# Kernel optimization log

Hardware: AMD Instinct MI355X
Metric: run time of the kernel (lower is better)

The kernel has to match this reference:

```python
import jax, jax.numpy as jnp
import numpy as np

STEPS = 30
BATCH = 1048576
HIDDEN = 32


def setup_inputs() -> dict:
    key = jax.random.key(0)
    k_s, k_w1, k_b1, k_w2, k_b2 = jax.random.split(key, 5)
    return {
        "S": jax.random.normal(k_s, (BATCH, STEPS), dtype=jnp.float32),
        "W1": jax.random.normal(k_w1, (3, HIDDEN), dtype=jnp.float32) * (1.0 / np.sqrt(3.0)),
        "b1": jax.random.normal(k_b1, (HIDDEN,), dtype=jnp.float32) * 0.01,
        "W2": jax.random.normal(k_w2, (HIDDEN, 1), dtype=jnp.float32) * (1.0 / np.sqrt(HIDDEN)),
        "b2": jax.random.normal(k_b2, (1,), dtype=jnp.float32) * 0.01,
        "a_init": jnp.zeros((1,), dtype=jnp.float32),
    }


def reference(S, W1, b1, W2, b2, a_init):
    B = S.shape[0]
    h0 = jnp.zeros((B, 1), dtype=S.dtype)
    d0 = jnp.broadcast_to(a_init.reshape(1, 1), (B, 1))  # a_init.expand(batch, 1)

    def step(carry, s_t):
        h, d_prev = carry
        x = jnp.concatenate([s_t[:, None], d_prev, h], axis=1)  # (B, 3)
        hidden = jax.nn.relu(x @ W1 + b1)                        # (B, 32)
        d = hidden @ W2 + b2                                     # (B, 1)
        h_new = 0.8 * h + 0.2 * d
        return (h_new, d), d

    # scan over time: S.T has shape (steps, B)
    (_, _), deltas = jax.lax.scan(step, (h0, d0), S.T)
    # deltas: (steps, B, 1) -> (B, steps)
    return jnp.transpose(deltas[:, :, 0], (1, 0))
```

## Files before the change

kernel.cpp:

```cpp
#include <hip/hip_runtime.h>

#define STEPS 30
#define HID 32
#define HALF_H 16
#define TPB 256
#define EPB (TPB / 2)
#define LDS_STRIDE (STEPS + 1)

__global__ __launch_bounds__(TPB, 4) void hedge_kernel(
    const float* __restrict__ S,
    const float* __restrict__ W1,
    const float* __restrict__ b1,
    const float* __restrict__ W2,
    const float* __restrict__ b2,
    const float* __restrict__ a_init,
    float* __restrict__ out)
{
    __shared__ float tile[EPB * LDS_STRIDE];
    const int tid  = threadIdx.x;
    const int half = tid & 1;
    const int el   = tid >> 1;
    const long long base = (long long)blockIdx.x * (EPB * STEPS);

    #pragma unroll
    for (int k = 0; k < (EPB * STEPS) / TPB; ++k) {
        int idx = tid + k * TPB;
        float v = S[base + idx];
        int row = idx / STEPS;
        int col = idx - row * STEPS;
        tile[row * LDS_STRIDE + col] = v;
    }

    const int j0 = half * HALF_H;
    float wa[HALF_H], wc[HALF_H], we[HALF_H], wb[HALF_H], w2[HALF_H];
    #pragma unroll
    for (int q = 0; q < HALF_H / 4; ++q) {
        float4 va = ((const float4*)(W1 + 0 * HID + j0))[q];
        float4 vc = ((const float4*)(W1 + 1 * HID + j0))[q];
        float4 ve = ((const float4*)(W1 + 2 * HID + j0))[q];
        float4 vb = ((const float4*)(b1 + j0))[q];
        float4 v2 = ((const float4*)(W2 + j0))[q];
        wa[4*q+0]=va.x; wa[4*q+1]=va.y; wa[4*q+2]=va.z; wa[4*q+3]=va.w;
        wc[4*q+0]=vc.x; wc[4*q+1]=vc.y; wc[4*q+2]=vc.z; wc[4*q+3]=vc.w;
        we[4*q+0]=ve.x; we[4*q+1]=ve.y; we[4*q+2]=ve.z; we[4*q+3]=ve.w;
        wb[4*q+0]=vb.x; wb[4*q+1]=vb.y; wb[4*q+2]=vb.z; wb[4*q+3]=vb.w;
        w2[4*q+0]=v2.x; w2[4*q+1]=v2.y; w2[4*q+2]=v2.z; w2[4*q+3]=v2.w;
    }
    const float bias2 = b2[0];
    float d = a_init[0];
    float h = 0.0f;
    __syncthreads();

    float* my = &tile[el * LDS_STRIDE];
    #pragma unroll
    for (int t = 0; t < STEPS; ++t) {
        const float s = my[t];
        float a0 = 0.f, a1 = 0.f, a2 = 0.f, a3 = 0.f;
        #pragma unroll
        for (int j = 0; j < HALF_H; j += 4) {
            float t0 = fmaf(wa[j+0], s, fmaf(wc[j+0], d, fmaf(we[j+0], h, wb[j+0])));
            float t1 = fmaf(wa[j+1], s, fmaf(wc[j+1], d, fmaf(we[j+1], h, wb[j+1])));
            float t2 = fmaf(wa[j+2], s, fmaf(wc[j+2], d, fmaf(we[j+2], h, wb[j+2])));
            float t3 = fmaf(wa[j+3], s, fmaf(wc[j+3], d, fmaf(we[j+3], h, wb[j+3])));
            a0 = fmaf(fmaxf(t0, 0.f), w2[j+0], a0);
            a1 = fmaf(fmaxf(t1, 0.f), w2[j+1], a1);
            a2 = fmaf(fmaxf(t2, 0.f), w2[j+2], a2);
            a3 = fmaf(fmaxf(t3, 0.f), w2[j+3], a3);
        }
        float acc = (a0 + a1) + (a2 + a3);
        acc += __shfl_xor(acc, 1, 64);
        const float dn = bias2 + acc;
        h = fmaf(0.2f, dn, 0.8f * h);
        d = dn;
        if (!half) my[t] = dn;
    }
    __syncthreads();

    #pragma unroll
    for (int k = 0; k < (EPB * STEPS) / TPB; ++k) {
        int idx = tid + k * TPB;
        int row = idx / STEPS;
        int col = idx - row * STEPS;
        out[base + idx] = tile[row * LDS_STRIDE + col];
    }
}

extern "C" void kernel_launch(void* const* d_in, const int* in_sizes, int n_in,
                              void* d_out, int out_size, void* d_ws, size_t ws_size,
                              hipStream_t stream) {
    const float* S      = (const float*)d_in[0];
    const float* W1     = (const float*)d_in[1];
    const float* b1     = (const float*)d_in[2];
    const float* W2     = (const float*)d_in[3];
    const float* b2     = (const float*)d_in[4];
    const float* a_init = (const float*)d_in[5];
    float* out = (float*)d_out;

    const int batch = in_sizes[0] / STEPS;
    const int grid  = batch / EPB;
    hedge_kernel<<<grid, TPB, 0, stream>>>(S, W1, b1, W2, b2, a_init, out);
}
```

Before: 275.0 us.

## Compute first layer with fp16 MFMA 32x32x16 instead of scalar FMAs

Replaces the per-thread scalar first-layer FMAs with one fp16 MFMA per step per wave. Each wave handles 32 batch elements, with hidden units spread across the MFMA output rows, and lane pairs combine partial sums via shuffle. This moves the dominant arithmetic onto the matrix cores. It adds fp16 rounding of the weights, the inputs and the recurrent state, which can compound over 30 steps and hurt accuracy. Each step now also pays serial MFMA latency inside the recurrence.

Result: faster. 259.6 us (-5.6%).

```diff
diff --git a/kernel.cpp b/kernel.cpp
--- a/kernel.cpp
+++ b/kernel.cpp
@@ -2,10 +2,17 @@
 
 #define STEPS 30
 #define HID 32
-#define HALF_H 16
 #define TPB 256
-#define EPB (TPB / 2)
+#define EPB 128
 #define LDS_STRIDE (STEPS + 1)
+
+typedef float f32x16 __attribute__((ext_vector_type(16)));
+typedef __fp16 h8 __attribute__((ext_vector_type(8)));
+typedef unsigned int u32x4 __attribute__((ext_vector_type(4)));
+
+static __device__ __forceinline__ unsigned int pkrtz_u32(float x, float y) {
+    return __builtin_bit_cast(unsigned int, __builtin_amdgcn_cvt_pkrtz(x, y));
+}
 
 __global__ __launch_bounds__(TPB, 4) void hedge_kernel(
     const float* __restrict__ S,
@@ -18,8 +25,8 @@
 {
     __shared__ float tile[EPB * LDS_STRIDE];
     const int tid  = threadIdx.x;
-    const int half = tid & 1;
-    const int el   = tid >> 1;
+    const int lane = tid & 63;
+    const int wv   = tid >> 6;
     const long long base = (long long)blockIdx.x * (EPB * STEPS);
 
     #pragma unroll
@@ -31,48 +38,59 @@
         tile[row * LDS_STRIDE + col] = v;
     }
 
-    const int j0 = half * HALF_H;
-    float wa[HALF_H], wc[HALF_H], we[HALF_H], wb[HALF_H], w2[HALF_H];
+    const int j = lane & 31;
+    const float wbf = b1[j];
+    const float waf = W1[0 * HID + j];
+    const float wcf = W1[1 * HID + j];
+    const float wef = W1[2 * HID + j];
+    u32x4 av;
+    if (lane < 32) {
+        av[0] = pkrtz_u32(wbf, waf);
+        av[1] = pkrtz_u32(wcf, wef);
+        av[2] = 0u; av[3] = 0u;
+    } else {
+        av[0] = 0u; av[1] = 0u; av[2] = 0u; av[3] = 0u;
+    }
+    const h8 afrag = __builtin_bit_cast(h8, av);
+
+    const int rbase = 4 * (lane >> 5);
+    float w2r[16];
     #pragma unroll
-    for (int q = 0; q < HALF_H / 4; ++q) {
-        float4 va = ((const float4*)(W1 + 0 * HID + j0))[q];
-        float4 vc = ((const float4*)(W1 + 1 * HID + j0))[q];
-        float4 ve = ((const float4*)(W1 + 2 * HID + j0))[q];
-        float4 vb = ((const float4*)(b1 + j0))[q];
-        float4 v2 = ((const float4*)(W2 + j0))[q];
-        wa[4*q+0]=va.x; wa[4*q+1]=va.y; wa[4*q+2]=va.z; wa[4*q+3]=va.w;
-        wc[4*q+0]=vc.x; wc[4*q+1]=vc.y; wc[4*q+2]=vc.z; wc[4*q+3]=vc.w;
-        we[4*q+0]=ve.x; we[4*q+1]=ve.y; we[4*q+2]=ve.z; we[4*q+3]=ve.w;
-        wb[4*q+0]=vb.x; wb[4*q+1]=vb.y; wb[4*q+2]=vb.z; wb[4*q+3]=vb.w;
-        w2[4*q+0]=v2.x; w2[4*q+1]=v2.y; w2[4*q+2]=v2.z; w2[4*q+3]=v2.w;
-    }
+    for (int r = 0; r < 16; ++r)
+        w2r[r] = W2[(r & 3) + 8 * (r >> 2) + rbase];
+
     const float bias2 = b2[0];
     float d = a_init[0];
     float h = 0.0f;
+    const f32x16 zero16 = {0.f};
     __syncthreads();
 
-    float* my = &tile[el * LDS_STRIDE];
+    float* my = &tile[(32 * wv + (lane & 31)) * LDS_STRIDE];
     #pragma unroll
     for (int t = 0; t < STEPS; ++t) {
         const float s = my[t];
+        u32x4 bv;
+        bv[0] = pkrtz_u32(1.0f, s);
+        bv[1] = pkrtz_u32(d, h);
+        bv[2] = bv[0]; bv[3] = bv[1];
+        const h8 bfrag = __builtin_bit_cast(h8, bv);
+
+        const f32x16 P = __builtin_amdgcn_mfma_f32_32x32x16_f16(afrag, bfrag, zero16, 0, 0, 0);
+
         float a0 = 0.f, a1 = 0.f, a2 = 0.f, a3 = 0.f;
         #pragma unroll
-        for (int j = 0; j < HALF_H; j += 4) {
-            float t0 = fmaf(wa[j+0], s, fmaf(wc[j+0], d, fmaf(we[j+0], h, wb[j+0])));
-            float t1 = fmaf(wa[j+1], s, fmaf(wc[j+1], d, fmaf(we[j+1], h, wb[j+1])));
-            float t2 = fmaf(wa[j+2], s, fmaf(wc[j+2], d, fmaf(we[j+2], h, wb[j+2])));
-            float t3 = fmaf(wa[j+3], s, fmaf(wc[j+3], d, fmaf(we[j+3], h, wb[j+3])));
-            a0 = fmaf(fmaxf(t0, 0.f), w2[j+0], a0);
-            a1 = fmaf(fmaxf(t1, 0.f), w2[j+1], a1);
-            a2 = fmaf(fmaxf(t2, 0.f), w2[j+2], a2);
-            a3 = fmaf(fmaxf(t3, 0.f), w2[j+3], a3);
+        for (int r = 0; r < 16; r += 4) {
+            a0 = fmaf(w2r[r + 0], fmaxf(P[r + 0], 0.f), a0);
+            a1 = fmaf(w2r[r + 1], fmaxf(P[r + 1], 0.f), a1);
+            a2 = fmaf(w2r[r + 2], fmaxf(P[r + 2], 0.f), a2);
+            a3 = fmaf(w2r[r + 3], fmaxf(P[r + 3], 0.f), a3);
         }
-        float acc = (a0 + a1) + (a2 + a3);
-        acc += __shfl_xor(acc, 1, 64);
-        const float dn = bias2 + acc;
+        float part = (a0 + a1) + (a2 + a3);
+        part += __shfl_xor(part, 32);
+        const float dn = bias2 + part;
         h = fmaf(0.2f, dn, 0.8f * h);
         d = dn;
-        if (!half) my[t] = dn;
+        my[t] = dn;
     }
     __syncthreads();
 
```
